# Kernel optimization log

Measured on AMD Instinct MI355X. Metric: run time of the kernel, lower is better.

Reference implementation:

```python
import jax, jax.numpy as jnp
import numpy as np

EMBED = 1024
TOKLEN = 100
NLAYERS = 24
TOKDIM = 256
MLP = int(EMBED * 0.125)  # 128, hardcoded mlp_ratio=0.125
SEQ, BATCH = 4097, 8  # 4096 patch tokens + 1 cls token


def setup_inputs() -> dict:
    key = jax.random.key(0)
    ks = jax.random.split(key, 8)
    s = 0.02  # kaiming-like small init scale
    return {
        "x": jax.random.normal(ks[0], (SEQ, BATCH, EMBED), jnp.float32),
        "layer": 3,
        "A": jax.random.normal(ks[1], (1, TOKLEN, EMBED), jnp.float32) * s,
        "B": jax.random.normal(ks[2], (NLAYERS, EMBED, TOKDIM), jnp.float32) * s,
        "Wd": jax.random.normal(ks[3], (MLP, TOKDIM), jnp.float32) * s,
        "bd": jnp.zeros((MLP,), jnp.float32),
        "Wu": jax.random.normal(ks[4], (EMBED, MLP), jnp.float32) * s,
        "bu": jnp.zeros((EMBED,), jnp.float32),
        "Wt": jax.random.normal(ks[5], (EMBED, EMBED), jnp.float32) * s,
        "bt": jnp.zeros((EMBED,), jnp.float32),
        "Wf": jax.random.normal(ks[6], (EMBED, EMBED), jnp.float32) * s,
        "bf": jnp.zeros((EMBED,), jnp.float32),
        "scale": jnp.asarray(0.001, jnp.float32),
    }


def reference(x, layer, A, B, Wd, bd, Wu, bu, Wt, bt, Wf, bf, scale):
    # batch_first=False, has_cls_token=True, evp_feature=None (module defaults)
    cls_tok, body = x[:1], x[1:]              # [1,b,c], [n,b,c]
    # get_tokens(layer): tokens = A[0] @ up(gelu(down(B[layer])))
    Bl = B[layer]                              # [c, token_dim]
    fB = jax.nn.gelu(Bl @ Wd.T + bd, approximate=False) @ Wu.T + bu  # [c, c]
    tokens = A[0] @ fB                         # [m, c]
    # forward_delta_feat: cross-attention to the m=100 learned tokens
    attn = jax.nn.softmax(
        jnp.einsum("nbc,mc->nbm", body, tokens) * (EMBED ** -0.5), axis=-1
    )                                          # [n, b, m]
    tfeat = tokens @ Wt.T + bt                 # mlp_token2feat, [m, c]
    delta = jnp.einsum("nbm,mc->nbc", attn, tfeat)
    delta = (delta + body) @ Wf.T + bf         # mlp_delta_f
    out = body + delta * scale                 # scaled residual fuse
    return jnp.concatenate([cls_tok, out], axis=0)
```

## Files before the change

### kernel.cpp

```cpp
#include <hip/hip_runtime.h>
#include <stdint.h>

#define EMBED 1024
#define TOKLEN 100
#define TOKDIM 256
#define MLPD 128
#define KEXT 1152

typedef float f32x4 __attribute__((ext_vector_type(4)));
typedef __bf16 bf16x8 __attribute__((ext_vector_type(8)));

__device__ __forceinline__ unsigned short f2bf(float f) {
  unsigned int u = __float_as_uint(f);
  u += 0x7fffu + ((u >> 16) & 1);
  return (unsigned short)(u >> 16);
}
__device__ __forceinline__ float bf2f(unsigned short h) {
  return __uint_as_float(((unsigned int)h) << 16);
}
__device__ __forceinline__ void async16(const void* g, void* l) {
  __builtin_amdgcn_global_load_lds(
      (const __attribute__((address_space(1))) unsigned int*)g,
      (__attribute__((address_space(3))) unsigned int*)l, 16, 0, 0);
}



__global__ void k_gelu(const float* __restrict__ B, const int* __restrict__ layer,
                       const float* __restrict__ Wd, const float* __restrict__ bd,
                       float* __restrict__ G) {
  int idx = blockIdx.x * 256 + threadIdx.x;
  int c = idx >> 7, j = idx & 127;
  const float* bl = B + ((size_t)layer[0] * EMBED + c) * TOKDIM;
  const float* wd = Wd + (size_t)j * TOKDIM;
  float a0 = 0.f, a1 = 0.f, a2 = 0.f, a3 = 0.f;
  for (int k = 0; k < TOKDIM; k += 4) {
    float4 a = *(const float4*)(bl + k);
    float4 b = *(const float4*)(wd + k);
    a0 += a.x * b.x; a1 += a.y * b.y; a2 += a.z * b.z; a3 += a.w * b.w;
  }
  float v = a0 + a1 + a2 + a3 + bd[j];
  G[idx] = 0.5f * v * (1.f + erff(v * 0.70710678118654752440f));
}

__global__ void k_ag(const float* __restrict__ A, const float* __restrict__ G,
                     float* __restrict__ AG, float* __restrict__ asum) {
  int m = blockIdx.x, j = threadIdx.x;
  const float* a = A + (size_t)m * EMBED;
  float acc = 0.f, s = 0.f;
  for (int c = 0; c < EMBED; ++c) acc += a[c] * G[(size_t)c * MLPD + j];
  AG[(size_t)m * MLPD + j] = acc;
  for (int c = j; c < EMBED; c += 128) s += a[c];
  __shared__ float red[128];
  red[j] = s; __syncthreads();
  for (int w = 64; w > 0; w >>= 1) { if (j < w) red[j] += red[j + w]; __syncthreads(); }
  if (j == 0) asum[m] = red[0];
}

__global__ void k_tokens(const float* __restrict__ AG, const float* __restrict__ asum,
                         const float* __restrict__ Wu, const float* __restrict__ bu,
                         unsigned short* __restrict__ tokbf) {
  int m = blockIdx.x, t = threadIdx.x;
  if (m >= TOKLEN) {
    #pragma unroll
    for (int i = 0; i < 4; ++i) tokbf[(size_t)m * EMBED + t * 4 + i] = 0;
    return;
  }
  __shared__ float ag[MLPD];
  __shared__ float as_s;
  if (t < MLPD) ag[t] = AG[(size_t)m * MLPD + t];
  if (t == 0) as_s = asum[m];
  __syncthreads();
  #pragma unroll
  for (int i = 0; i < 4; ++i) {
    int e = t * 4 + i;
    const float* wu = Wu + (size_t)e * MLPD;
    float a0 = 0.f, a1 = 0.f, a2 = 0.f, a3 = 0.f;
    for (int j = 0; j < MLPD; j += 4) {
      float4 w = *(const float4*)(wu + j);
      a0 += w.x * ag[j]; a1 += w.y * ag[j + 1]; a2 += w.z * ag[j + 2]; a3 += w.w * ag[j + 3];
    }
    tokbf[(size_t)m * EMBED + e] = f2bf(a0 + a1 + a2 + a3 + as_s * bu[e]);
  }
}

__global__ void k_wprep(const float* __restrict__ Wf, const float* __restrict__ Wt,
                        const float* __restrict__ bt,
                        unsigned short* __restrict__ Bt, unsigned short* __restrict__ wfbf,
                        unsigned short* __restrict__ wtbf, float* __restrict__ wfbt) {
  int e = blockIdx.x, t = threadIdx.x;
  float4 v = *(const float4*)(Wf + (size_t)e * EMBED + t * 4);
  uint2 u;
  u.x = (unsigned int)f2bf(v.x) | ((unsigned int)f2bf(v.y) << 16);
  u.y = (unsigned int)f2bf(v.z) | ((unsigned int)f2bf(v.w) << 16);
  *(uint2*)(Bt + (size_t)e * KEXT + t * 4) = u;
  *(uint2*)(wfbf + (size_t)e * EMBED + t * 4) = u;
  if (t < 28) Bt[(size_t)e * KEXT + 1124 + t] = 0;
  float4 w = *(const float4*)(Wt + (size_t)e * EMBED + t * 4);
  uint2 u2;
  u2.x = (unsigned int)f2bf(w.x) | ((unsigned int)f2bf(w.y) << 16);
  u2.y = (unsigned int)f2bf(w.z) | ((unsigned int)f2bf(w.w) << 16);
  *(uint2*)(wtbf + (size_t)e * EMBED + t * 4) = u2;
  float4 b = *(const float4*)(bt + t * 4);
  __shared__ float red[256];
  red[t] = v.x * b.x + v.y * b.y + v.z * b.z + v.w * b.w;
  __syncthreads();
  for (int s = 128; s > 0; s >>= 1) { if (t < s) red[t] += red[t + s]; __syncthreads(); }
  if (t == 0) wfbt[e] = red[0];
}

__global__ void k_cls(const float* __restrict__ x, float* __restrict__ out) {
  int i = blockIdx.x * 256 + threadIdx.x;
  ((float4*)out)[i] = ((const float4*)x)[i];
}


__global__ void __launch_bounds__(256) k_tf1(const unsigned short* __restrict__ tokbf,
                                             const unsigned short* __restrict__ wtbf,
                                             unsigned short* __restrict__ tfeatbf) {
  __shared__ unsigned short As[2][128 * 64];
  __shared__ unsigned short Bs[2][128 * 64];
  const int tid = threadIdx.x;
  const int wave = tid >> 6, lane = tid & 63;
  const int l15 = lane & 15, quad = lane >> 4;
  const int srow = lane >> 3, schunk = lane & 7;
  const int col0 = blockIdx.x * 128;
  const int wr = (wave >> 1) * 64, wc = (wave & 1) * 64;

  f32x4 acc[4][4];
  const f32x4 zero = {0.f, 0.f, 0.f, 0.f};
  #pragma unroll
  for (int i = 0; i < 4; ++i)
    #pragma unroll
    for (int j = 0; j < 4; ++j) acc[i][j] = zero;

  auto stage = [&](int buf, int kt) {
    const int k0 = kt * 64;
    #pragma unroll
    for (int i = 0; i < 4; ++i) {
      const int r = i * 32 + wave * 8;
      async16(tokbf + (size_t)(r + srow) * EMBED + k0 + (schunk ^ srow) * 8, &As[buf][r * 64]);
      async16(wtbf + (size_t)(col0 + r + srow) * EMBED + k0 + (schunk ^ srow) * 8, &Bs[buf][r * 64]);
    }
  };
  auto compute = [&](int buf) {
    #pragma unroll
    for (int ks = 0; ks < 2; ++ks) {
      const int sw = ((ks * 4 + quad) ^ (l15 & 7)) * 8;
      bf16x8 a[4], b[4];
      #pragma unroll
      for (int i = 0; i < 4; ++i)
        a[i] = *(const bf16x8*)&As[buf][(wr + i * 16 + l15) * 64 + sw];
      #pragma unroll
      for (int j = 0; j < 4; ++j)
        b[j] = *(const bf16x8*)&Bs[buf][(wc + j * 16 + l15) * 64 + sw];
      #pragma unroll
      for (int i = 0; i < 4; ++i)
        #pragma unroll
        for (int j = 0; j < 4; ++j)
          acc[i][j] = __builtin_amdgcn_mfma_f32_16x16x32_bf16(a[i], b[j], acc[i][j], 0, 0, 0);
    }
  };

  stage(0, 0);
  asm volatile("s_waitcnt vmcnt(0)" ::: "memory");
  __syncthreads();
  int cur = 0;
  for (int kt = 0; kt < 16; ++kt) {
    if (kt < 15) stage(cur ^ 1, kt + 1);
    compute(cur);
    asm volatile("s_waitcnt vmcnt(0)" ::: "memory");
    __syncthreads();
    cur ^= 1;
  }
  #pragma unroll
  for (int j = 0; j < 4; ++j) {
    const int e = col0 + wc + j * 16 + l15;
    #pragma unroll
    for (int i = 0; i < 4; ++i) {
      const int mb = wr + i * 16 + quad * 4;
      #pragma unroll
      for (int r = 0; r < 4; ++r)
        tfeatbf[(size_t)(mb + r) * EMBED + e] = f2bf(acc[i][j][r]);
    }
  }
}

__global__ void __launch_bounds__(256) k_tf2(const unsigned short* __restrict__ wfbf,
                                             const unsigned short* __restrict__ tfeatbf,
                                             const float* __restrict__ wfbt,
                                             unsigned short* __restrict__ Bt) {
  __shared__ unsigned short As[2][128 * 64];
  __shared__ unsigned short Bs[2][128 * 64];
  const int tid = threadIdx.x;
  const int wave = tid >> 6, lane = tid & 63;
  const int l15 = lane & 15, quad = lane >> 4;
  const int srow = lane >> 3, schunk = lane & 7;
  const int row0 = blockIdx.x * 128;
  const int wr = (wave >> 1) * 64, wc = (wave & 1) * 64;

  f32x4 acc[4][4];
  const f32x4 zero = {0.f, 0.f, 0.f, 0.f};
  #pragma unroll
  for (int i = 0; i < 4; ++i)
    #pragma unroll
    for (int j = 0; j < 4; ++j) acc[i][j] = zero;

  auto stage = [&](int buf, int kt) {
    const int k0 = kt * 64;
    #pragma unroll
    for (int i = 0; i < 4; ++i) {
      const int r = i * 32 + wave * 8;
      async16(wfbf + (size_t)(row0 + r + srow) * EMBED + k0 + (schunk ^ srow) * 8, &As[buf][r * 64]);
      async16(tfeatbf + (size_t)(r + srow) * EMBED + k0 + (schunk ^ srow) * 8, &Bs[buf][r * 64]);
    }
  };
  auto compute = [&](int buf) {
    #pragma unroll
    for (int ks = 0; ks < 2; ++ks) {
      const int sw = ((ks * 4 + quad) ^ (l15 & 7)) * 8;
      bf16x8 a[4], b[4];
      #pragma unroll
      for (int i = 0; i < 4; ++i)
        a[i] = *(const bf16x8*)&As[buf][(wr + i * 16 + l15) * 64 + sw];
      #pragma unroll
      for (int j = 0; j < 4; ++j)
        b[j] = *(const bf16x8*)&Bs[buf][(wc + j * 16 + l15) * 64 + sw];
      #pragma unroll
      for (int i = 0; i < 4; ++i)
        #pragma unroll
        for (int j = 0; j < 4; ++j)
          acc[i][j] = __builtin_amdgcn_mfma_f32_16x16x32_bf16(a[i], b[j], acc[i][j], 0, 0, 0);
    }
  };

  stage(0, 0);
  asm volatile("s_waitcnt vmcnt(0)" ::: "memory");
  __syncthreads();
  int cur = 0;
  for (int kt = 0; kt < 16; ++kt) {
    if (kt < 15) stage(cur ^ 1, kt + 1);
    compute(cur);
    asm volatile("s_waitcnt vmcnt(0)" ::: "memory");
    __syncthreads();
    cur ^= 1;
  }
  #pragma unroll
  for (int j = 0; j < 4; ++j) {
    const int m = wc + j * 16 + l15;
    #pragma unroll
    for (int i = 0; i < 4; ++i) {
      const int eb = row0 + wr + i * 16 + quad * 4;
      #pragma unroll
      for (int r = 0; r < 4; ++r)
        Bt[(size_t)(eb + r) * KEXT + 1024 + m] = f2bf(acc[i][j][r] + wfbt[eb + r]);
    }
  }
}

__global__ void __launch_bounds__(256) k_attn(const float* __restrict__ x,
                                              const unsigned short* __restrict__ tokbf,
                                              unsigned short* __restrict__ Aext) {
  __shared__ __align__(16) unsigned short smem[2 * 128 * 72 + 2 * 128 * 64];
  const int tid = threadIdx.x;
  const int wave = tid >> 6, lane = tid & 63;
  const int l15 = lane & 15, quad = lane >> 4;
  const int srow = lane >> 3, schunk = lane & 7;
  const int row0 = blockIdx.x * 128;
  const int trow = tid >> 1, thalf = tid & 1;
  const float* body = x + 8 * EMBED;
  const float* gxbase = body + (size_t)(row0 + trow) * EMBED + thalf * 32;

  f32x4 acc[2][8];
  const f32x4 zero = {0.f, 0.f, 0.f, 0.f};
  #pragma unroll
  for (int i = 0; i < 2; ++i)
    #pragma unroll
    for (int j = 0; j < 8; ++j) acc[i][j] = zero;

  float4 v[8];

  auto regload = [&](int kt) {
    const float* gx = gxbase + kt * 64;
    #pragma unroll
    for (int q = 0; q < 8; ++q) v[q] = *(const float4*)(gx + q * 4);
  };
  auto tsstage = [&](int buf, int kt) {
    unsigned short* Ts = smem + 2 * 128 * 72 + buf * (128 * 64);
    const int k0 = kt * 64;
    #pragma unroll
    for (int i = 0; i < 4; ++i) {
      const int r = i * 32 + wave * 8;
      async16(tokbf + (size_t)(r + srow) * EMBED + k0 + (schunk ^ srow) * 8, &Ts[r * 64]);
    }
  };
  auto convwrite = [&](int buf, int kt) {
    unsigned short* As = smem + buf * (128 * 72);
    unsigned int pk[16];
    #pragma unroll
    for (int q = 0; q < 8; ++q) {
      pk[q * 2]     = (unsigned int)f2bf(v[q].x) | ((unsigned int)f2bf(v[q].y) << 16);
      pk[q * 2 + 1] = (unsigned int)f2bf(v[q].z) | ((unsigned int)f2bf(v[q].w) << 16);
    }
    unsigned int* lw = (unsigned int*)&As[trow * 72 + thalf * 32];
    unsigned int* gw = (unsigned int*)(Aext + (size_t)(row0 + trow) * KEXT + kt * 64 + thalf * 32);
    #pragma unroll
    for (int q = 0; q < 4; ++q) {
      uint4 u; u.x = pk[q*4]; u.y = pk[q*4+1]; u.z = pk[q*4+2]; u.w = pk[q*4+3];
      ((uint4*)lw)[q] = u;
      ((uint4*)gw)[q] = u;
    }
  };
  auto compute = [&](int buf) {
    unsigned short* As = smem + buf * (128 * 72);
    unsigned short* Ts = smem + 2 * 128 * 72 + buf * (128 * 64);
    #pragma unroll
    for (int ks = 0; ks < 2; ++ks) {
      const int sw = ((ks * 4 + quad) ^ (l15 & 7)) * 8;
      bf16x8 a[2], b[8];
      #pragma unroll
      for (int i = 0; i < 2; ++i)
        a[i] = *(const bf16x8*)&As[(wave * 32 + i * 16 + l15) * 72 + ks * 32 + quad * 8];
      #pragma unroll
      for (int j = 0; j < 8; ++j)
        b[j] = *(const bf16x8*)&Ts[(j * 16 + l15) * 64 + sw];
      #pragma unroll
      for (int i = 0; i < 2; ++i)
        #pragma unroll
        for (int j = 0; j < 8; ++j)
          acc[i][j] = __builtin_amdgcn_mfma_f32_16x16x32_bf16(a[i], b[j], acc[i][j], 0, 0, 0);
    }
  };

  regload(0); tsstage(0, 0);
  asm volatile("s_waitcnt vmcnt(0)" ::: "memory");
  convwrite(0, 0);
  __syncthreads();
  int cur = 0;
  for (int kt = 0; kt < 16; ++kt) {
    if (kt < 15) { regload(kt + 1); tsstage(cur ^ 1, kt + 1); }
    compute(cur);
    if (kt < 15) {
      asm volatile("s_waitcnt vmcnt(0)" ::: "memory");
      convwrite(cur ^ 1, kt + 1);
    }
    __syncthreads();
    cur ^= 1;
  }

  unsigned short* Sc = smem;
  #pragma unroll
  for (int i = 0; i < 2; ++i) {
    #pragma unroll
    for (int r = 0; r < 4; ++r) {
      float mx = -1e30f;
      #pragma unroll
      for (int j = 0; j < 8; ++j) {
        const int c = j * 16 + l15;
        const float vv = acc[i][j][r] * 0.03125f;
        if (c < TOKLEN) mx = fmaxf(mx, vv);
      }
      #pragma unroll
      for (int d = 1; d < 16; d <<= 1) mx = fmaxf(mx, __shfl_xor(mx, d));
      float sm = 0.f;
      #pragma unroll
      for (int j = 0; j < 8; ++j) {
        const int c = j * 16 + l15;
        if (c < TOKLEN) sm += __expf(acc[i][j][r] * 0.03125f - mx);
      }
      #pragma unroll
      for (int d = 1; d < 16; d <<= 1) sm += __shfl_xor(sm, d);
      const float inv = 1.f / sm;
      const int row = wave * 32 + i * 16 + quad * 4 + r;
      #pragma unroll
      for (int j = 0; j < 8; ++j) {
        const int c = j * 16 + l15;
        const float p = (c < TOKLEN) ? __expf(acc[i][j][r] * 0.03125f - mx) * inv : 0.f;
        Sc[row * 128 + c] = f2bf(p);
      }
    }
  }
  __syncthreads();
  {
    const int r = tid >> 1, h = tid & 1;
    const uint4* src = (const uint4*)(Sc + r * 128 + h * 64);
    uint4* dst = (uint4*)(Aext + (size_t)(row0 + r) * KEXT + 1024 + h * 64);
    dst[0] = src[0]; dst[1] = src[1]; dst[2] = src[2]; dst[3] = src[3];
  }
}


#define MAIN_MFMA16(MH, KS)                                                     \
    acc[(MH)*4+0][0] = __builtin_amdgcn_mfma_f32_16x16x32_bf16(pa0##KS, pb0##KS, acc[(MH)*4+0][0], 0, 0, 0); \
    acc[(MH)*4+1][0] = __builtin_amdgcn_mfma_f32_16x16x32_bf16(pa1##KS, pb0##KS, acc[(MH)*4+1][0], 0, 0, 0); \
    acc[(MH)*4+2][0] = __builtin_amdgcn_mfma_f32_16x16x32_bf16(pa2##KS, pb0##KS, acc[(MH)*4+2][0], 0, 0, 0); \
    acc[(MH)*4+3][0] = __builtin_amdgcn_mfma_f32_16x16x32_bf16(pa3##KS, pb0##KS, acc[(MH)*4+3][0], 0, 0, 0); \
    acc[(MH)*4+0][1] = __builtin_amdgcn_mfma_f32_16x16x32_bf16(pa0##KS, pb1##KS, acc[(MH)*4+0][1], 0, 0, 0); \
    acc[(MH)*4+1][1] = __builtin_amdgcn_mfma_f32_16x16x32_bf16(pa1##KS, pb1##KS, acc[(MH)*4+1][1], 0, 0, 0); \
    acc[(MH)*4+2][1] = __builtin_amdgcn_mfma_f32_16x16x32_bf16(pa2##KS, pb1##KS, acc[(MH)*4+2][1], 0, 0, 0); \
    acc[(MH)*4+3][1] = __builtin_amdgcn_mfma_f32_16x16x32_bf16(pa3##KS, pb1##KS, acc[(MH)*4+3][1], 0, 0, 0); \
    acc[(MH)*4+0][2] = __builtin_amdgcn_mfma_f32_16x16x32_bf16(pa0##KS, pb2##KS, acc[(MH)*4+0][2], 0, 0, 0); \
    acc[(MH)*4+1][2] = __builtin_amdgcn_mfma_f32_16x16x32_bf16(pa1##KS, pb2##KS, acc[(MH)*4+1][2], 0, 0, 0); \
    acc[(MH)*4+2][2] = __builtin_amdgcn_mfma_f32_16x16x32_bf16(pa2##KS, pb2##KS, acc[(MH)*4+2][2], 0, 0, 0); \
    acc[(MH)*4+3][2] = __builtin_amdgcn_mfma_f32_16x16x32_bf16(pa3##KS, pb2##KS, acc[(MH)*4+3][2], 0, 0, 0); \
    acc[(MH)*4+0][3] = __builtin_amdgcn_mfma_f32_16x16x32_bf16(pa0##KS, pb3##KS, acc[(MH)*4+0][3], 0, 0, 0); \
    acc[(MH)*4+1][3] = __builtin_amdgcn_mfma_f32_16x16x32_bf16(pa1##KS, pb3##KS, acc[(MH)*4+1][3], 0, 0, 0); \
    acc[(MH)*4+2][3] = __builtin_amdgcn_mfma_f32_16x16x32_bf16(pa2##KS, pb3##KS, acc[(MH)*4+2][3], 0, 0, 0); \
    acc[(MH)*4+3][3] = __builtin_amdgcn_mfma_f32_16x16x32_bf16(pa3##KS, pb3##KS, acc[(MH)*4+3][3], 0, 0, 0);

#define MAIN_PHASE(S, MH, LOADB)                                                \
  do {                                                                          \
    const int sw0 = (quad ^ (l15 & 7)) * 8;                                     \
    const int sw1 = ((4 + quad) ^ (l15 & 7)) * 8;                               \
    const unsigned short* Ah = &Ab[S][wm][0];                                   \
    if (LOADB) {                                                                \
      const unsigned short* Bh = &Bb[S][bh][0];                                 \
      pb0_0 = *(const bf16x8*)&Bh[(brb + 0 * 16 + l15) * 64 + sw0];             \
      pb1_0 = *(const bf16x8*)&Bh[(brb + 1 * 16 + l15) * 64 + sw0];             \
      pb2_0 = *(const bf16x8*)&Bh[(brb + 2 * 16 + l15) * 64 + sw0];             \
      pb3_0 = *(const bf16x8*)&Bh[(brb + 3 * 16 + l15) * 64 + sw0];             \
      pb0_1 = *(const bf16x8*)&Bh[(brb + 0 * 16 + l15) * 64 + sw1];             \
      pb1_1 = *(const bf16x8*)&Bh[(brb + 1 * 16 + l15) * 64 + sw1];             \
      pb2_1 = *(const bf16x8*)&Bh[(brb + 2 * 16 + l15) * 64 + sw1];             \
      pb3_1 = *(const bf16x8*)&Bh[(brb + 3 * 16 + l15) * 64 + sw1];             \
    }                                                                           \
    bf16x8 pa0_0 = *(const bf16x8*)&Ah[((MH)*64 + 0 * 16 + l15) * 64 + sw0];    \
    bf16x8 pa1_0 = *(const bf16x8*)&Ah[((MH)*64 + 1 * 16 + l15) * 64 + sw0];    \
    bf16x8 pa2_0 = *(const bf16x8*)&Ah[((MH)*64 + 2 * 16 + l15) * 64 + sw0];    \
    bf16x8 pa3_0 = *(const bf16x8*)&Ah[((MH)*64 + 3 * 16 + l15) * 64 + sw0];    \
    bf16x8 pa0_1 = *(const bf16x8*)&Ah[((MH)*64 + 0 * 16 + l15) * 64 + sw1];    \
    bf16x8 pa1_1 = *(const bf16x8*)&Ah[((MH)*64 + 1 * 16 + l15) * 64 + sw1];    \
    bf16x8 pa2_1 = *(const bf16x8*)&Ah[((MH)*64 + 2 * 16 + l15) * 64 + sw1];    \
    bf16x8 pa3_1 = *(const bf16x8*)&Ah[((MH)*64 + 3 * 16 + l15) * 64 + sw1];    \
    asm volatile("s_barrier" ::: "memory");                                     \
    __builtin_amdgcn_s_setprio(1);                                              \
    MAIN_MFMA16(MH, _0)                                                         \
    MAIN_MFMA16(MH, _1)                                                         \
    __builtin_amdgcn_s_setprio(0);                                              \
    asm volatile("s_barrier" ::: "memory");                                     \
  } while (0)

#define ISSUE_TILE(KT, S)                                                       \
  do {                                                                          \
    const int k0_ = (KT) * 64;                                                  \
    _Pragma("unroll")                                                           \
    for (int h_ = 0; h_ < 2; ++h_) {                                            \
      _Pragma("unroll")                                                         \
      for (int r2_ = 0; r2_ < 2; ++r2_) {                                       \
        const int rb_ = r2_ * 64 + w8;                                          \
        async16(Aext + (size_t)(row0 + h_ * 128 + rb_ + srow) * KEXT + k0_ + (schunk ^ srow) * 8, \
                &Ab[S][h_][rb_ * 64]);                                          \
        async16(Bt + (size_t)(col0 + h_ * 128 + rb_ + srow) * KEXT + k0_ + (schunk ^ srow) * 8,   \
                &Bb[S][h_][rb_ * 64]);                                          \
      }                                                                         \
    }                                                                           \
  } while (0)

__global__ void __launch_bounds__(512) k_main(const unsigned short* __restrict__ Aext,
                                              const unsigned short* __restrict__ Bt,
                                              const float* __restrict__ x,
                                              const float* __restrict__ bfv,
                                              const float* __restrict__ scale,
                                              float* __restrict__ out) {
  __shared__ unsigned short Ab[2][2][128 * 64];
  __shared__ unsigned short Bb[2][2][128 * 64];
  const int tid = threadIdx.x;
  const int w = tid >> 6, lane = tid & 63;
  const int l15 = lane & 15, quad = lane >> 4;
  const int srow = lane >> 3, schunk = lane & 7;
  const int w8 = w * 8;
  const int wm = w >> 2, wn = w & 3;
  const int bh = wn >> 1, brb = (wn & 1) * 64;

  const int xcd = blockIdx.x & 7, slot = blockIdx.x >> 3;
  const int rt = (slot >> 2) * 8 + xcd;
  const int ct = slot & 3;
  const int row0 = rt * 256;
  const int col0 = ct * 256;

  f32x4 acc[8][4];
  const f32x4 zero = {0.f, 0.f, 0.f, 0.f};
  #pragma unroll
  for (int i = 0; i < 8; ++i)
    #pragma unroll
    for (int j = 0; j < 4; ++j) acc[i][j] = zero;

  bf16x8 pb0_0, pb1_0, pb2_0, pb3_0, pb0_1, pb1_1, pb2_1, pb3_1;

  ISSUE_TILE(0, 0);
  #pragma unroll 1
  for (int i = 0; i < 9; ++i) {
    asm volatile("s_waitcnt vmcnt(0)" ::: "memory");
    asm volatile("s_barrier" ::: "memory");
    ISSUE_TILE(2 * i + 1, 1);
    MAIN_PHASE(0, 0, 1);
    MAIN_PHASE(0, 1, 0);
    asm volatile("s_waitcnt vmcnt(0)" ::: "memory");
    asm volatile("s_barrier" ::: "memory");
    if (i < 8) ISSUE_TILE(2 * i + 2, 0);
    MAIN_PHASE(1, 0, 1);
    MAIN_PHASE(1, 1, 0);
  }

  const float s = scale[0];
  #pragma unroll
  for (int mf = 0; mf < 8; ++mf) {
    const int rb = row0 + wm * 128 + mf * 16 + quad * 4;
    #pragma unroll
    for (int nf = 0; nf < 4; ++nf) {
      const int c = col0 + wn * 64 + nf * 16 + l15;
      const float bfc = bfv[c];
      #pragma unroll
      for (int r = 0; r < 4; ++r) {
        const size_t idx = (size_t)(rb + r + 8) * EMBED + c;
        out[idx] = x[idx] + (acc[mf][nf][r] + bfc) * s;
      }
    }
  }
}

extern "C" void kernel_launch(void* const* d_in, const int* in_sizes, int n_in,
                              void* d_out, int out_size, void* d_ws, size_t ws_size,
                              hipStream_t stream) {
  const float* x     = (const float*)d_in[0];
  const int*   layer = (const int*)d_in[1];
  const float* A     = (const float*)d_in[2];
  const float* B     = (const float*)d_in[3];
  const float* Wd    = (const float*)d_in[4];
  const float* bd    = (const float*)d_in[5];
  const float* Wu    = (const float*)d_in[6];
  const float* bu    = (const float*)d_in[7];
  const float* Wt    = (const float*)d_in[8];
  const float* bt    = (const float*)d_in[9];
  const float* Wf    = (const float*)d_in[10];
  const float* bf    = (const float*)d_in[11];
  const float* scale = (const float*)d_in[12];
  float* out = (float*)d_out;

  char* ws = (char*)d_ws;
  unsigned short* Aext    = (unsigned short*)(ws + 0);
  unsigned short* wtbf    = (unsigned short*)(ws + 0);
  unsigned short* wfbf    = (unsigned short*)(ws + 2097152);
  unsigned short* Bt_     = (unsigned short*)(ws + 75497472);
  unsigned short* tokbf   = (unsigned short*)(ws + 77856768);
  float*          G       = (float*)(ws + 78118912);
  float*          AG      = (float*)(ws + 78643200);
  float*          asum    = (float*)(ws + 78694400);
  float*          wfbt    = (float*)(ws + 78694912);
  unsigned short* tfeatbf = (unsigned short*)(ws + 78699008);

  k_gelu  <<<512, 256, 0, stream>>>(B, layer, Wd, bd, G);
  k_ag    <<<100, 128, 0, stream>>>(A, G, AG, asum);
  k_tokens<<<128, 256, 0, stream>>>(AG, asum, Wu, bu, tokbf);
  k_wprep <<<1024, 256, 0, stream>>>(Wf, Wt, bt, Bt_, wfbf, wtbf, wfbt);
  k_tf1   <<<8, 256, 0, stream>>>(tokbf, wtbf, tfeatbf);
  k_tf2   <<<8, 256, 0, stream>>>(wfbf, tfeatbf, wfbt, Bt_);
  k_cls   <<<8, 256, 0, stream>>>(x, out);
  k_attn  <<<256, 256, 0, stream>>>(x, tokbf, Aext);
  k_main  <<<512, 512, 0, stream>>>(Aext, Bt_, x, bf, scale, out);
}
```

Before: 533.9 us.

## Deepen prefetch pipelines in attention and main GEMM, fold cls copy into wprep

The cls-token copy kernel is removed and folded into the weight-prep kernel, saving one launch. In k_attn, activations are now register double-buffered two k-steps ahead, with partial vmcnt waits instead of full drains, and the kernel gets launch_bounds(256,2). In k_main, two tiles are issued before the loop and the next tile is issued after compute with vmcnt(8), so global loads overlap the MFMA phases instead of draining before each barrier. This adds register pressure and depends on exact counts of outstanding loads, so miscounting vmcnt could cause races.

```diff
diff --git a/kernel.cpp b/kernel.cpp
--- a/kernel.cpp
+++ b/kernel.cpp
@@ -85,10 +85,15 @@
 }
 
 __global__ void k_wprep(const float* __restrict__ Wf, const float* __restrict__ Wt,
-                        const float* __restrict__ bt,
+                        const float* __restrict__ bt, const float* __restrict__ x,
+                        float* __restrict__ out,
                         unsigned short* __restrict__ Bt, unsigned short* __restrict__ wfbf,
                         unsigned short* __restrict__ wtbf, float* __restrict__ wfbt) {
   int e = blockIdx.x, t = threadIdx.x;
+  if (e < 8) {
+    int i = e * 256 + t;
+    ((float4*)out)[i] = ((const float4*)x)[i];
+  }
   float4 v = *(const float4*)(Wf + (size_t)e * EMBED + t * 4);
   uint2 u;
   u.x = (unsigned int)f2bf(v.x) | ((unsigned int)f2bf(v.y) << 16);
@@ -109,11 +114,6 @@
   if (t == 0) wfbt[e] = red[0];
 }
 
-__global__ void k_cls(const float* __restrict__ x, float* __restrict__ out) {
-  int i = blockIdx.x * 256 + threadIdx.x;
-  ((float4*)out)[i] = ((const float4*)x)[i];
-}
-
 
 __global__ void __launch_bounds__(256) k_tf1(const unsigned short* __restrict__ tokbf,
                                              const unsigned short* __restrict__ wtbf,
@@ -258,9 +258,9 @@
   }
 }
 
-__global__ void __launch_bounds__(256) k_attn(const float* __restrict__ x,
-                                              const unsigned short* __restrict__ tokbf,
-                                              unsigned short* __restrict__ Aext) {
+__global__ void __launch_bounds__(256, 2) k_attn(const float* __restrict__ x,
+                                                 const unsigned short* __restrict__ tokbf,
+                                                 unsigned short* __restrict__ Aext) {
   __shared__ __align__(16) unsigned short smem[2 * 128 * 72 + 2 * 128 * 64];
   const int tid = threadIdx.x;
   const int wave = tid >> 6, lane = tid & 63;
@@ -278,9 +278,9 @@
     #pragma unroll
     for (int j = 0; j < 8; ++j) acc[i][j] = zero;
 
-  float4 v[8];
-
-  auto regload = [&](int kt) {
+  float4 va[8], vb[8];
+
+  auto regload = [&](int kt, float4* v) {
     const float* gx = gxbase + kt * 64;
     #pragma unroll
     for (int q = 0; q < 8; ++q) v[q] = *(const float4*)(gx + q * 4);
@@ -294,7 +294,7 @@
       async16(tokbf + (size_t)(r + srow) * EMBED + k0 + (schunk ^ srow) * 8, &Ts[r * 64]);
     }
   };
-  auto convwrite = [&](int buf, int kt) {
+  auto convwrite = [&](int buf, int kt, const float4* v) {
     unsigned short* As = smem + buf * (128 * 72);
     unsigned int pk[16];
     #pragma unroll
@@ -332,20 +332,29 @@
     }
   };
 
-  regload(0); tsstage(0, 0);
+  regload(0, va); tsstage(0, 0);
   asm volatile("s_waitcnt vmcnt(0)" ::: "memory");
-  convwrite(0, 0);
-  __syncthreads();
-  int cur = 0;
+  convwrite(0, 0, va);
+  regload(1, vb);
+  asm volatile("s_waitcnt lgkmcnt(0)" ::: "memory");
+  asm volatile("s_barrier" ::: "memory");
+
+  #pragma unroll 1
   for (int kt = 0; kt < 16; ++kt) {
-    if (kt < 15) { regload(kt + 1); tsstage(cur ^ 1, kt + 1); }
+    const int cur = kt & 1;
+    if (kt < 15) tsstage(cur ^ 1, kt + 1);
+    if (kt < 14) {
+      if (cur) regload(kt + 2, vb); else regload(kt + 2, va);
+    }
     compute(cur);
     if (kt < 15) {
-      asm volatile("s_waitcnt vmcnt(0)" ::: "memory");
-      convwrite(cur ^ 1, kt + 1);
-    }
-    __syncthreads();
-    cur ^= 1;
+      if (kt < 14) asm volatile("s_waitcnt vmcnt(8)" ::: "memory");
+      else         asm volatile("s_waitcnt vmcnt(0)" ::: "memory");
+      if (cur) convwrite(cur ^ 1, kt + 1, va);
+      else     convwrite(cur ^ 1, kt + 1, vb);
+      asm volatile("s_waitcnt lgkmcnt(0)" ::: "memory");
+    }
+    asm volatile("s_barrier" ::: "memory");
   }
 
   unsigned short* Sc = smem;
@@ -488,18 +497,27 @@
   bf16x8 pb0_0, pb1_0, pb2_0, pb3_0, pb0_1, pb1_1, pb2_1, pb3_1;
 
   ISSUE_TILE(0, 0);
+  ISSUE_TILE(1, 1);
+  asm volatile("s_waitcnt vmcnt(8)" ::: "memory");
+  asm volatile("s_barrier" ::: "memory");
   #pragma unroll 1
   for (int i = 0; i < 9; ++i) {
-    asm volatile("s_waitcnt vmcnt(0)" ::: "memory");
-    asm volatile("s_barrier" ::: "memory");
-    ISSUE_TILE(2 * i + 1, 1);
     MAIN_PHASE(0, 0, 1);
     MAIN_PHASE(0, 1, 0);
-    asm volatile("s_waitcnt vmcnt(0)" ::: "memory");
+    if (i < 8) {
+      ISSUE_TILE(2 * i + 2, 0);
+      asm volatile("s_waitcnt vmcnt(8)" ::: "memory");
+    } else {
+      asm volatile("s_waitcnt vmcnt(0)" ::: "memory");
+    }
     asm volatile("s_barrier" ::: "memory");
-    if (i < 8) ISSUE_TILE(2 * i + 2, 0);
     MAIN_PHASE(1, 0, 1);
     MAIN_PHASE(1, 1, 0);
+    if (i < 8) {
+      ISSUE_TILE(2 * i + 3, 1);
+      asm volatile("s_waitcnt vmcnt(8)" ::: "memory");
+      asm volatile("s_barrier" ::: "memory");
+    }
   }
 
   const float s = scale[0];
@@ -552,10 +570,9 @@
   k_gelu  <<<512, 256, 0, stream>>>(B, layer, Wd, bd, G);
   k_ag    <<<100, 128, 0, stream>>>(A, G, AG, asum);
   k_tokens<<<128, 256, 0, stream>>>(AG, asum, Wu, bu, tokbf);
-  k_wprep <<<1024, 256, 0, stream>>>(Wf, Wt, bt, Bt_, wfbf, wtbf, wfbt);
+  k_wprep <<<1024, 256, 0, stream>>>(Wf, Wt, bt, x, out, Bt_, wfbf, wtbf, wfbt);
   k_tf1   <<<8, 256, 0, stream>>>(tokbf, wtbf, tfeatbf);
   k_tf2   <<<8, 256, 0, stream>>>(wfbf, tfeatbf, wfbt, Bt_);
-  k_cls   <<<8, 256, 0, stream>>>(x, out);
   k_attn  <<<256, 256, 0, stream>>>(x, tokbf, Aext);
   k_main  <<<512, 512, 0, stream>>>(Aext, Bt_, x, bf, scale, out);
 }
```

Measured after the change: 528.1 us. About the same (-1.1%).
